# Kernel tuning notes

Measured on AMD Instinct MI355X. Metric: run time of the kernel, lower is better.

## Reference

```python
import jax, jax.numpy as jnp
import numpy as np

N_NODES = 20000
N_EDGES = 640000
NODE_DIM = 128
EDGE_DIM = 64
HID = 128  # must equal NODE_DIM (index_add_ into zeros_like(node_feat) in the original)
EPS = 1e-8


def setup_inputs() -> dict:
    key = jax.random.key(0)
    ks = jax.random.split(key, 16)
    s = 0.05
    return {
        "node_feat": jax.random.normal(ks[0], (N_NODES, NODE_DIM), jnp.float32),
        "edge_index": jax.random.randint(ks[1], (2, N_EDGES), 0, N_NODES, jnp.int32),
        "edge_attr": jax.random.normal(ks[2], (N_EDGES, EDGE_DIM), jnp.float32),
        "coords": jax.random.normal(ks[3], (N_NODES, 3), jnp.float32),
        # edge_mlp: Linear(2*node+edge -> hid), SiLU, Linear(hid -> hid), SiLU
        "eW1": jax.random.normal(ks[4], (2 * NODE_DIM + EDGE_DIM, HID), jnp.float32) * s,
        "eb1": jnp.zeros((HID,), jnp.float32),
        "eW2": jax.random.normal(ks[5], (HID, HID), jnp.float32) * s,
        "eb2": jnp.zeros((HID,), jnp.float32),
        # node_mlp: Linear(node+hid -> hid), SiLU, Linear(hid -> node)
        "nW1": jax.random.normal(ks[6], (NODE_DIM + HID, HID), jnp.float32) * s,
        "nb1": jnp.zeros((HID,), jnp.float32),
        "nW2": jax.random.normal(ks[7], (HID, NODE_DIM), jnp.float32) * s,
        "nb2": jnp.zeros((NODE_DIM,), jnp.float32),
        # coord_mlp: Linear(hid -> hid//2), SiLU, Linear(hid//2 -> 1)
        "cW1": jax.random.normal(ks[8], (HID, HID // 2), jnp.float32) * s,
        "cb1": jnp.zeros((HID // 2,), jnp.float32),
        "cW2": jax.random.normal(ks[9], (HID // 2, 1), jnp.float32) * s,
        "cb2": jnp.zeros((1,), jnp.float32),
    }


def reference(node_feat, edge_index, edge_attr, coords,
              eW1, eb1, eW2, eb2, nW1, nb1, nW2, nb2, cW1, cb1, cW2, cb2):
    silu = jax.nn.silu
    src, dst = edge_index[0], edge_index[1]

    # edge messages: gather -> concat -> 2-layer MLP (SiLU after both layers)
    edge_feat = jnp.concatenate([node_feat[src], node_feat[dst], edge_attr], axis=-1)  # [E, 2*node+edge]
    edge_message = silu(silu(edge_feat @ eW1 + eb1) @ eW2 + eb2)  # [E, hid]

    # aggregate messages per destination node (index_add_)
    aggr_message = jax.ops.segment_sum(edge_message, dst, num_segments=N_NODES)  # [N, hid]

    # node update (residual)
    node_input = jnp.concatenate([node_feat, aggr_message], axis=-1)
    node_update = silu(node_input @ nW1 + nb1) @ nW2 + nb2
    updated_nodes = node_feat + node_update

    # coordinate update: per-edge scalar weight times unit direction, scattered to dst
    coord_weights = silu(edge_message @ cW1 + cb1) @ cW2 + cb2  # [E, 1]
    coord_diff = coords[src] - coords[dst]  # [E, 3]
    coord_diff = coord_diff / (jnp.linalg.norm(coord_diff, axis=-1, keepdims=True) + EPS)
    coord_update = jax.ops.segment_sum(coord_weights * coord_diff, dst, num_segments=N_NODES)
    updated_coords = coords + coord_update

    return updated_nodes, updated_coords
```

## Files before the change

kernel.cpp:

```cpp
#include <hip/hip_runtime.h>
#include <math.h>

#define N_NODES 20000
#define N_EDGES 640000
#define D 128
#define ED 64
#define EPS 1e-8f
#define MT 64

#define FSTRIDE 328
#define HSTRIDE 136
#define MSG_OFF (MT * HSTRIDE)
#define LDS_SHORTS (MT * FSTRIDE)

#define NSTRIDE 264

#define EW2_OFF 40960
#define CW1_OFF 57344
#define NW1_OFF 65536
#define NW2_OFF 98304
#define NFBF_OFF 114688

typedef __attribute__((ext_vector_type(8))) short bf16x8;
typedef __attribute__((ext_vector_type(16))) float f32x16;
typedef __attribute__((ext_vector_type(2))) float f32x2;

__device__ __forceinline__ float silu_f(float x) { return x / (1.0f + __expf(-x)); }

__device__ __forceinline__ short f2bf(float f) {
    union { float f; unsigned u; } v; v.f = f;
    unsigned r = v.u + 0x7FFFu + ((v.u >> 16) & 1u);
    return (short)(r >> 16);
}
__device__ __forceinline__ float bf2f(short s) {
    union { unsigned u; float f; } v;
    v.u = ((unsigned)(unsigned short)s) << 16;
    return v.f;
}

#define SWZ_ADD(x, imm) (x + __int_as_float( \
    __builtin_amdgcn_ds_swizzle(__float_as_int(x), imm)))

__global__ __launch_bounds__(256)
void prep_kernel(const float* __restrict__ eW1, const float* __restrict__ eW2,
                 const float* __restrict__ cW1, const float* __restrict__ nW1,
                 const float* __restrict__ nW2,
                 const float* __restrict__ node_feat,
                 const float* __restrict__ coords,
                 short* __restrict__ wsf, short* __restrict__ nfbf,
                 float* __restrict__ nodes_io, float* __restrict__ out_coords) {
    const int t = blockIdx.x * blockDim.x + threadIdx.x;
    const int nthr = gridDim.x * blockDim.x;

    if (t < 224 * 64) {
        int f = t >> 6, lane = t & 63;
        const float* src; int kc, nt, ncol; size_t dst;
        if (f < 80)       {              src = eW1; kc = f >> 2;  nt = f & 3;  ncol = 128; dst = (size_t)f * 512; }
        else if (f < 112) { int g=f-80;  src = eW2; kc = g >> 2;  nt = g & 3;  ncol = 128; dst = EW2_OFF + (size_t)g * 512; }
        else if (f < 128) { int g=f-112; src = cW1; kc = g >> 1;  nt = g & 1;  ncol = 64;  dst = CW1_OFF + (size_t)g * 512; }
        else if (f < 192) { int g=f-128; src = nW1; kc = g >> 2;  nt = g & 3;  ncol = 128; dst = NW1_OFF + (size_t)g * 512; }
        else              { int g=f-192; src = nW2; kc = g >> 2;  nt = g & 3;  ncol = 128; dst = NW2_OFF + (size_t)g * 512; }
        int col = nt * 32 + (lane & 31);
        int k0  = kc * 16 + (lane >> 5) * 8;
        bf16x8 o;
        #pragma unroll
        for (int j = 0; j < 8; ++j) o[j] = f2bf(src[(size_t)(k0 + j) * ncol + col]);
        *(bf16x8*)&wsf[dst + (size_t)lane * 8] = o;
    }
    for (int idx = t; idx < N_NODES * D / 8; idx += nthr) {
        const float* s = node_feat + (size_t)idx * 8;
        float4 f0 = *(const float4*)s, f1 = *(const float4*)(s + 4);
        bf16x8 pk;
        pk[0]=f2bf(f0.x); pk[1]=f2bf(f0.y); pk[2]=f2bf(f0.z); pk[3]=f2bf(f0.w);
        pk[4]=f2bf(f1.x); pk[5]=f2bf(f1.y); pk[6]=f2bf(f1.z); pk[7]=f2bf(f1.w);
        *(bf16x8*)&nfbf[(size_t)idx * 8] = pk;
    }
    for (int idx = t; idx < N_NODES * D / 4; idx += nthr) {
        float4 z; z.x = 0.f; z.y = 0.f; z.z = 0.f; z.w = 0.f;
        *(float4*)&nodes_io[(size_t)idx * 4] = z;
    }
    for (int idx = t; idx < N_NODES * 3; idx += nthr)
        out_coords[idx] = coords[idx];
}

__global__ __launch_bounds__(256, 3)
void edge_kernel(const short* __restrict__ nfbf,
                 const int* __restrict__ edge_index,
                 const float* __restrict__ edge_attr,
                 const float* __restrict__ coords,
                 const float* __restrict__ eb1, const float* __restrict__ eb2,
                 const float* __restrict__ cb1, const float* __restrict__ cW2,
                 const float* __restrict__ cb2,
                 const short* __restrict__ wsf,
                 float* __restrict__ aggr_nodes, float* __restrict__ out_coords) {
    __shared__ __align__(16) short lds[LDS_SHORTS];
    __shared__ int s_src[MT], s_dst[MT];
    __shared__ float s_wgt[MT];

    const int tid = threadIdx.x;
    const int E0 = blockIdx.x * MT;

    {
        int e = tid >> 2, p = tid & 3;
        int esrc = edge_index[E0 + e];
        int edst = edge_index[N_EDGES + E0 + e];
        if (p == 0) { s_src[e] = esrc; s_dst[e] = edst; }
        const short* srow = nfbf + (size_t)esrc * D;
        const short* drow = nfbf + (size_t)edst * D;
        short* frow = &lds[e * FSTRIDE];
        #pragma unroll
        for (int c = 0; c < 4; ++c)
            *(bf16x8*)&frow[c * 32 + p * 8] = *(const bf16x8*)&srow[c * 32 + p * 8];
        #pragma unroll
        for (int c = 0; c < 4; ++c)
            *(bf16x8*)&frow[128 + c * 32 + p * 8] = *(const bf16x8*)&drow[c * 32 + p * 8];
        const float* arow = edge_attr + (size_t)(E0 + e) * ED + p * 16;
        float4 a0 = *(const float4*)&arow[0], a1 = *(const float4*)&arow[4];
        float4 a2 = *(const float4*)&arow[8], a3 = *(const float4*)&arow[12];
        bf16x8 p0, p1;
        p0[0]=f2bf(a0.x); p0[1]=f2bf(a0.y); p0[2]=f2bf(a0.z); p0[3]=f2bf(a0.w);
        p0[4]=f2bf(a1.x); p0[5]=f2bf(a1.y); p0[6]=f2bf(a1.z); p0[7]=f2bf(a1.w);
        p1[0]=f2bf(a2.x); p1[1]=f2bf(a2.y); p1[2]=f2bf(a2.z); p1[3]=f2bf(a2.w);
        p1[4]=f2bf(a3.x); p1[5]=f2bf(a3.y); p1[6]=f2bf(a3.z); p1[7]=f2bf(a3.w);
        *(bf16x8*)&frow[256 + p * 16]     = p0;
        *(bf16x8*)&frow[256 + p * 16 + 8] = p1;
    }
    __syncthreads();

    const int lane  = tid & 63;
    const int wv    = tid >> 6;
    const int m0    = (wv >> 1) * 32;
    const int n0q   = wv & 1;
    const int l31   = lane & 31;
    const int khalf = lane >> 5;

    const bf16x8* W1 = (const bf16x8*)wsf;
    const bf16x8* W2 = (const bf16x8*)(wsf + EW2_OFF);
    const bf16x8* W3 = (const bf16x8*)(wsf + CW1_OFF);

    {
        f32x16 acc0, acc1;
        #pragma unroll
        for (int r = 0; r < 16; ++r) { acc0[r] = 0.f; acc1[r] = 0.f; }
        #pragma unroll
        for (int kc = 0; kc < 20; ++kc) {
            bf16x8 a  = *(const bf16x8*)&lds[(m0 + l31) * FSTRIDE + kc * 16 + khalf * 8];
            bf16x8 b0 = W1[(kc * 4 + n0q * 2 + 0) * 64 + lane];
            bf16x8 b1 = W1[(kc * 4 + n0q * 2 + 1) * 64 + lane];
            acc0 = __builtin_amdgcn_mfma_f32_32x32x16_bf16(a, b0, acc0, 0, 0, 0);
            acc1 = __builtin_amdgcn_mfma_f32_32x32x16_bf16(a, b1, acc1, 0, 0, 0);
        }
        __syncthreads();
        #pragma unroll
        for (int nt = 0; nt < 2; ++nt) {
            f32x16 A = nt ? acc1 : acc0;
            int n = n0q * 64 + nt * 32 + l31;
            float bb = eb1[n];
            #pragma unroll
            for (int r = 0; r < 16; ++r) {
                int row = (r & 3) + 8 * (r >> 2) + 4 * khalf;
                lds[(m0 + row) * HSTRIDE + n] = f2bf(silu_f(A[r] + bb));
            }
        }
    }
    __syncthreads();

    {
        f32x16 acc0, acc1;
        #pragma unroll
        for (int r = 0; r < 16; ++r) { acc0[r] = 0.f; acc1[r] = 0.f; }
        #pragma unroll
        for (int kc = 0; kc < 8; ++kc) {
            bf16x8 a  = *(const bf16x8*)&lds[(m0 + l31) * HSTRIDE + kc * 16 + khalf * 8];
            bf16x8 b0 = W2[(kc * 4 + n0q * 2 + 0) * 64 + lane];
            bf16x8 b1 = W2[(kc * 4 + n0q * 2 + 1) * 64 + lane];
            acc0 = __builtin_amdgcn_mfma_f32_32x32x16_bf16(a, b0, acc0, 0, 0, 0);
            acc1 = __builtin_amdgcn_mfma_f32_32x32x16_bf16(a, b1, acc1, 0, 0, 0);
        }
        #pragma unroll
        for (int nt = 0; nt < 2; ++nt) {
            f32x16 A = nt ? acc1 : acc0;
            int n = n0q * 64 + nt * 32 + l31;
            float bb = eb2[n];
            #pragma unroll
            for (int r = 0; r < 16; ++r) {
                int row = (r & 3) + 8 * (r >> 2) + 4 * khalf;
                lds[MSG_OFF + (m0 + row) * HSTRIDE + n] = f2bf(silu_f(A[r] + bb));
            }
        }
    }
    __syncthreads();

    {
        f32x16 c0, c1;
        #pragma unroll
        for (int r = 0; r < 16; ++r) { c0[r] = 0.f; c1[r] = 0.f; }
        #pragma unroll
        for (int kc = 0; kc < 8; ++kc) {
            bf16x8 a  = *(const bf16x8*)&lds[MSG_OFF + (m0 + l31) * HSTRIDE + kc * 16 + khalf * 8];
            bf16x8 b0 = W3[(kc * 2 + 0) * 64 + lane];
            bf16x8 b1 = W3[(kc * 2 + 1) * 64 + lane];
            c0 = __builtin_amdgcn_mfma_f32_32x32x16_bf16(a, b0, c0, 0, 0, 0);
            c1 = __builtin_amdgcn_mfma_f32_32x32x16_bf16(a, b1, c1, 0, 0, 0);
        }
        float b1a = cb1[l31], b1b = cb1[32 + l31];
        float w2a = cW2[l31], w2b = cW2[32 + l31];
        float part[16];
        #pragma unroll
        for (int r = 0; r < 16; ++r)
            part[r] = silu_f(c0[r] + b1a) * w2a + silu_f(c1[r] + b1b) * w2b;
        #pragma unroll
        for (int r = 0; r < 16; ++r) {
            part[r] = SWZ_ADD(part[r], 0x041F);
            part[r] = SWZ_ADD(part[r], 0x081F);
            part[r] = SWZ_ADD(part[r], 0x101F);
            part[r] = SWZ_ADD(part[r], 0x201F);
            part[r] = SWZ_ADD(part[r], 0x401F);
        }
        if (l31 == 0) {
            float cb2v = cb2[0];
            #pragma unroll
            for (int r = 0; r < 16; ++r)
                s_wgt[m0 + (r & 3) + 8 * (r >> 2) + 4 * khalf] = part[r] + cb2v;
        }
    }
    __syncthreads();

    if (tid < MT) {
        int e = tid;
        float wgt = s_wgt[e];
        int s = s_src[e], d = s_dst[e];
        float dx = coords[s * 3 + 0] - coords[d * 3 + 0];
        float dy = coords[s * 3 + 1] - coords[d * 3 + 1];
        float dz = coords[s * 3 + 2] - coords[d * 3 + 2];
        float inv = wgt / (sqrtf(dx * dx + dy * dy + dz * dz) + EPS);
        unsafeAtomicAdd(&out_coords[d * 3 + 0], dx * inv);
        unsafeAtomicAdd(&out_coords[d * 3 + 1], dy * inv);
        unsafeAtomicAdd(&out_coords[d * 3 + 2], dz * inv);
    }

#if __has_builtin(__builtin_amdgcn_global_atomic_fadd_v2f32)
    for (int idx = tid; idx < MT * D / 8; idx += 256) {
        int e = idx >> 4, c = idx & 15;
        bf16x8 m = *(const bf16x8*)&lds[MSG_OFF + e * HSTRIDE + c * 8];
        float* ap = &aggr_nodes[(size_t)s_dst[e] * D + c * 8];
        #pragma unroll
        for (int j = 0; j < 4; ++j) {
            f32x2 v; v[0] = bf2f(m[2 * j]); v[1] = bf2f(m[2 * j + 1]);
            __builtin_amdgcn_global_atomic_fadd_v2f32((f32x2*)(ap + 2 * j), v);
        }
    }
#else
    for (int idx = tid; idx < MT * D; idx += 256) {
        int e = idx >> 7, n = idx & 127;
        float v = bf2f(lds[MSG_OFF + e * HSTRIDE + n]);
        unsafeAtomicAdd(&aggr_nodes[(size_t)s_dst[e] * D + n], v);
    }
#endif
}

__global__ __launch_bounds__(256, 4)
void node_kernel(const float* __restrict__ node_feat,
                 const short* __restrict__ nfbf,
                 float* nodes_io,
                 const float* __restrict__ nb1, const float* __restrict__ nb2,
                 const short* __restrict__ wsf) {
    __shared__ __align__(16) short lds[MT * NSTRIDE];
    const int tid = threadIdx.x;
    const int N0 = blockIdx.x * MT;

    {
        int i = tid >> 2, p = tid & 3;
        int nid = N0 + i; if (nid > N_NODES - 1) nid = N_NODES - 1;
        const short* frow = nfbf + (size_t)nid * D;
        short* drow = &lds[i * NSTRIDE];
        #pragma unroll
        for (int c = 0; c < 4; ++c)
            *(bf16x8*)&drow[c * 32 + p * 8] = *(const bf16x8*)&frow[c * 32 + p * 8];
        const float* arow = nodes_io + (size_t)nid * D + p * 32;
        #pragma unroll
        for (int c = 0; c < 4; ++c) {
            float4 f0 = *(const float4*)&arow[c * 8];
            float4 f1 = *(const float4*)&arow[c * 8 + 4];
            bf16x8 pk;
            pk[0]=f2bf(f0.x); pk[1]=f2bf(f0.y); pk[2]=f2bf(f0.z); pk[3]=f2bf(f0.w);
            pk[4]=f2bf(f1.x); pk[5]=f2bf(f1.y); pk[6]=f2bf(f1.z); pk[7]=f2bf(f1.w);
            *(bf16x8*)&drow[128 + p * 32 + c * 8] = pk;
        }
    }
    __syncthreads();

    const int lane  = tid & 63;
    const int wv    = tid >> 6;
    const int m0    = (wv >> 1) * 32;
    const int n0q   = wv & 1;
    const int l31   = lane & 31;
    const int khalf = lane >> 5;

    const bf16x8* W1 = (const bf16x8*)(wsf + NW1_OFF);
    const bf16x8* W2 = (const bf16x8*)(wsf + NW2_OFF);

    {
        f32x16 acc0, acc1;
        #pragma unroll
        for (int r = 0; r < 16; ++r) { acc0[r] = 0.f; acc1[r] = 0.f; }
        #pragma unroll
        for (int kc = 0; kc < 16; ++kc) {
            bf16x8 a  = *(const bf16x8*)&lds[(m0 + l31) * NSTRIDE + kc * 16 + khalf * 8];
            bf16x8 b0 = W1[(kc * 4 + n0q * 2 + 0) * 64 + lane];
            bf16x8 b1 = W1[(kc * 4 + n0q * 2 + 1) * 64 + lane];
            acc0 = __builtin_amdgcn_mfma_f32_32x32x16_bf16(a, b0, acc0, 0, 0, 0);
            acc1 = __builtin_amdgcn_mfma_f32_32x32x16_bf16(a, b1, acc1, 0, 0, 0);
        }
        __syncthreads();
        #pragma unroll
        for (int nt = 0; nt < 2; ++nt) {
            f32x16 A = nt ? acc1 : acc0;
            int n = n0q * 64 + nt * 32 + l31;
            float bb = nb1[n];
            #pragma unroll
            for (int r = 0; r < 16; ++r) {
                int row = (r & 3) + 8 * (r >> 2) + 4 * khalf;
                lds[(m0 + row) * HSTRIDE + n] = f2bf(silu_f(A[r] + bb));
            }
        }
    }
    __syncthreads();

    {
        f32x16 acc0, acc1;
        #pragma unroll
        for (int r = 0; r < 16; ++r) { acc0[r] = 0.f; acc1[r] = 0.f; }
        #pragma unroll
        for (int kc = 0; kc < 8; ++kc) {
            bf16x8 a  = *(const bf16x8*)&lds[(m0 + l31) * HSTRIDE + kc * 16 + khalf * 8];
            bf16x8 b0 = W2[(kc * 4 + n0q * 2 + 0) * 64 + lane];
            bf16x8 b1 = W2[(kc * 4 + n0q * 2 + 1) * 64 + lane];
            acc0 = __builtin_amdgcn_mfma_f32_32x32x16_bf16(a, b0, acc0, 0, 0, 0);
            acc1 = __builtin_amdgcn_mfma_f32_32x32x16_bf16(a, b1, acc1, 0, 0, 0);
        }
        #pragma unroll
        for (int nt = 0; nt < 2; ++nt) {
            f32x16 A = nt ? acc1 : acc0;
            int n = n0q * 64 + nt * 32 + l31;
            float bb = nb2[n];
            #pragma unroll
            for (int r = 0; r < 16; ++r) {
                int row = (r & 3) + 8 * (r >> 2) + 4 * khalf;
                int nid = N0 + m0 + row;
                if (nid < N_NODES)
                    nodes_io[(size_t)nid * D + n] = A[r] + bb + node_feat[(size_t)nid * D + n];
            }
        }
    }
}

extern "C" void kernel_launch(void* const* d_in, const int* in_sizes, int n_in,
                              void* d_out, int out_size, void* d_ws, size_t ws_size,
                              hipStream_t stream) {
    const float* node_feat  = (const float*)d_in[0];
    const int*   edge_index = (const int*)d_in[1];
    const float* edge_attr  = (const float*)d_in[2];
    const float* coords     = (const float*)d_in[3];
    const float* eW1 = (const float*)d_in[4];
    const float* eb1 = (const float*)d_in[5];
    const float* eW2 = (const float*)d_in[6];
    const float* eb2 = (const float*)d_in[7];
    const float* nW1 = (const float*)d_in[8];
    const float* nb1 = (const float*)d_in[9];
    const float* nW2 = (const float*)d_in[10];
    const float* nb2 = (const float*)d_in[11];
    const float* cW1 = (const float*)d_in[12];
    const float* cb1 = (const float*)d_in[13];
    const float* cW2 = (const float*)d_in[14];
    const float* cb2 = (const float*)d_in[15];

    float* nodes_io   = (float*)d_out;
    float* out_coords = nodes_io + (size_t)N_NODES * D;
    short* wsf  = (short*)d_ws;
    short* nfbf = wsf + NFBF_OFF;

    prep_kernel<<<256, 256, 0, stream>>>(
        eW1, eW2, cW1, nW1, nW2, node_feat, coords,
        wsf, nfbf, nodes_io, out_coords);
    edge_kernel<<<N_EDGES / MT, 256, 0, stream>>>(
        nfbf, edge_index, edge_attr, coords,
        eb1, eb2, cb1, cW2, cb2, wsf, nodes_io, out_coords);
    node_kernel<<<(N_NODES + MT - 1) / MT, 256, 0, stream>>>(
        node_feat, nfbf, nodes_io, nb1, nb2, wsf);
}
```

Measured before the change: 635.1 us.

## Sort edges by destination and pre-reduce segments before atomic scatter

Adds a counting sort of edges by destination node: a histogram pass, a single-block scan and a scatter that builds a permutation. The edge kernel then processes edges in destination order and reduces runs of equal destination within each 64-edge tile before issuing atomics, for both node messages and coordinate updates. With about 32 edges per node, this should cut global atomic traffic substantially. The cost is three extra kernel launches, a serial one-block scan, gathered edge_attr reads through the permutation, and scalar atomics replacing the packed v2 atomics.

```diff
diff --git a/kernel.cpp b/kernel.cpp
--- a/kernel.cpp
+++ b/kernel.cpp
@@ -20,10 +20,11 @@
 #define NW1_OFF 65536
 #define NW2_OFF 98304
 #define NFBF_OFF 114688
+#define CSR_OFF  2674688
 
 typedef __attribute__((ext_vector_type(8))) short bf16x8;
+typedef __attribute__((ext_vector_type(4))) short bf16x4;
 typedef __attribute__((ext_vector_type(16))) float f32x16;
-typedef __attribute__((ext_vector_type(2))) float f32x2;
 
 __device__ __forceinline__ float silu_f(float x) { return x / (1.0f + __expf(-x)); }
 
@@ -48,6 +49,7 @@
                  const float* __restrict__ node_feat,
                  const float* __restrict__ coords,
                  short* __restrict__ wsf, short* __restrict__ nfbf,
+                 int* __restrict__ cnt,
                  float* __restrict__ nodes_io, float* __restrict__ out_coords) {
     const int t = blockIdx.x * blockDim.x + threadIdx.x;
     const int nthr = gridDim.x * blockDim.x;
@@ -79,13 +81,61 @@
         float4 z; z.x = 0.f; z.y = 0.f; z.z = 0.f; z.w = 0.f;
         *(float4*)&nodes_io[(size_t)idx * 4] = z;
     }
+    for (int idx = t; idx < N_NODES; idx += nthr) cnt[idx] = 0;
     for (int idx = t; idx < N_NODES * 3; idx += nthr)
         out_coords[idx] = coords[idx];
+}
+
+__global__ __launch_bounds__(256)
+void hist_kernel(const int* __restrict__ edge_index, int* __restrict__ cnt) {
+    int t = blockIdx.x * blockDim.x + threadIdx.x;
+    if (t < N_EDGES) atomicAdd(&cnt[edge_index[N_EDGES + t]], 1);
+}
+
+#define SCAN_T 1024
+#define SCAN_C 20
+__global__ __launch_bounds__(SCAN_T)
+void scan_kernel(const int* __restrict__ cnt, int* __restrict__ cursor) {
+    __shared__ int part[SCAN_T];
+    const int t = threadIdx.x;
+    const int base = t * SCAN_C;
+    int s = 0;
+    #pragma unroll
+    for (int i = 0; i < SCAN_C; ++i) {
+        int idx = base + i;
+        if (idx < N_NODES) s += cnt[idx];
+    }
+    part[t] = s;
+    __syncthreads();
+    for (int off = 1; off < SCAN_T; off <<= 1) {
+        int v = (t >= off) ? part[t - off] : 0;
+        __syncthreads();
+        part[t] += v;
+        __syncthreads();
+    }
+    int run = part[t] - s;
+    #pragma unroll
+    for (int i = 0; i < SCAN_C; ++i) {
+        int idx = base + i;
+        if (idx < N_NODES) { cursor[idx] = run; run += cnt[idx]; }
+    }
+}
+
+__global__ __launch_bounds__(256)
+void scatter_kernel(const int* __restrict__ edge_index,
+                    int* __restrict__ cursor, int* __restrict__ perm) {
+    int t = blockIdx.x * blockDim.x + threadIdx.x;
+    if (t < N_EDGES) {
+        int d = edge_index[N_EDGES + t];
+        int pos = atomicAdd(&cursor[d], 1);
+        perm[pos] = t;
+    }
 }
 
 __global__ __launch_bounds__(256, 3)
 void edge_kernel(const short* __restrict__ nfbf,
                  const int* __restrict__ edge_index,
+                 const int* __restrict__ perm,
                  const float* __restrict__ edge_attr,
                  const float* __restrict__ coords,
                  const float* __restrict__ eb1, const float* __restrict__ eb2,
@@ -96,25 +146,28 @@
     __shared__ __align__(16) short lds[LDS_SHORTS];
     __shared__ int s_src[MT], s_dst[MT];
     __shared__ float s_wgt[MT];
+    __shared__ float s_cv[MT][3];
+    __shared__ char s_segend[MT];
 
     const int tid = threadIdx.x;
     const int E0 = blockIdx.x * MT;
 
     {
-        int e = tid >> 2, p = tid & 3;
-        int esrc = edge_index[E0 + e];
-        int edst = edge_index[N_EDGES + E0 + e];
-        if (p == 0) { s_src[e] = esrc; s_dst[e] = edst; }
+        int i = tid >> 2, p = tid & 3;
+        int eid  = perm[E0 + i];
+        int esrc = edge_index[eid];
+        int edst = edge_index[N_EDGES + eid];
+        if (p == 0) { s_src[i] = esrc; s_dst[i] = edst; }
         const short* srow = nfbf + (size_t)esrc * D;
         const short* drow = nfbf + (size_t)edst * D;
-        short* frow = &lds[e * FSTRIDE];
+        short* frow = &lds[i * FSTRIDE];
         #pragma unroll
         for (int c = 0; c < 4; ++c)
             *(bf16x8*)&frow[c * 32 + p * 8] = *(const bf16x8*)&srow[c * 32 + p * 8];
         #pragma unroll
         for (int c = 0; c < 4; ++c)
             *(bf16x8*)&frow[128 + c * 32 + p * 8] = *(const bf16x8*)&drow[c * 32 + p * 8];
-        const float* arow = edge_attr + (size_t)(E0 + e) * ED + p * 16;
+        const float* arow = edge_attr + (size_t)eid * ED + p * 16;
         float4 a0 = *(const float4*)&arow[0], a1 = *(const float4*)&arow[4];
         float4 a2 = *(const float4*)&arow[8], a3 = *(const float4*)&arow[12];
         bf16x8 p0, p1;
@@ -127,6 +180,9 @@
     }
     __syncthreads();
 
+    if (tid < MT)
+        s_segend[tid] = (tid == MT - 1) || (s_dst[tid] != s_dst[tid + 1]);
+
     const int lane  = tid & 63;
     const int wv    = tid >> 6;
     const int m0    = (wv >> 1) * 32;
@@ -234,29 +290,51 @@
         float dy = coords[s * 3 + 1] - coords[d * 3 + 1];
         float dz = coords[s * 3 + 2] - coords[d * 3 + 2];
         float inv = wgt / (sqrtf(dx * dx + dy * dy + dz * dz) + EPS);
-        unsafeAtomicAdd(&out_coords[d * 3 + 0], dx * inv);
-        unsafeAtomicAdd(&out_coords[d * 3 + 1], dy * inv);
-        unsafeAtomicAdd(&out_coords[d * 3 + 2], dz * inv);
-    }
-
-#if __has_builtin(__builtin_amdgcn_global_atomic_fadd_v2f32)
-    for (int idx = tid; idx < MT * D / 8; idx += 256) {
-        int e = idx >> 4, c = idx & 15;
-        bf16x8 m = *(const bf16x8*)&lds[MSG_OFF + e * HSTRIDE + c * 8];
-        float* ap = &aggr_nodes[(size_t)s_dst[e] * D + c * 8];
-        #pragma unroll
-        for (int j = 0; j < 4; ++j) {
-            f32x2 v; v[0] = bf2f(m[2 * j]); v[1] = bf2f(m[2 * j + 1]);
-            __builtin_amdgcn_global_atomic_fadd_v2f32((f32x2*)(ap + 2 * j), v);
-        }
-    }
-#else
-    for (int idx = tid; idx < MT * D; idx += 256) {
-        int e = idx >> 7, n = idx & 127;
-        float v = bf2f(lds[MSG_OFF + e * HSTRIDE + n]);
-        unsafeAtomicAdd(&aggr_nodes[(size_t)s_dst[e] * D + n], v);
-    }
-#endif
+        s_cv[e][0] = dx * inv; s_cv[e][1] = dy * inv; s_cv[e][2] = dz * inv;
+    }
+    __syncthreads();
+
+    {
+        int q  = tid & 31;
+        int st = tid >> 5;
+        int c0 = q * 4;
+        float a0 = 0.f, a1 = 0.f, a2 = 0.f, a3 = 0.f;
+        #pragma unroll
+        for (int r = 0; r < 8; ++r) {
+            int e = st * 8 + r;
+            bf16x4 m = *(const bf16x4*)&lds[MSG_OFF + e * HSTRIDE + c0];
+            a0 += bf2f(m[0]); a1 += bf2f(m[1]); a2 += bf2f(m[2]); a3 += bf2f(m[3]);
+            if (s_segend[e]) {
+                float* ap = &aggr_nodes[(size_t)s_dst[e] * D + c0];
+                unsafeAtomicAdd(ap + 0, a0); unsafeAtomicAdd(ap + 1, a1);
+                unsafeAtomicAdd(ap + 2, a2); unsafeAtomicAdd(ap + 3, a3);
+                a0 = a1 = a2 = a3 = 0.f;
+            }
+        }
+        int elast = st * 8 + 7;
+        if (!s_segend[elast]) {
+            float* ap = &aggr_nodes[(size_t)s_dst[elast] * D + c0];
+            unsafeAtomicAdd(ap + 0, a0); unsafeAtomicAdd(ap + 1, a1);
+            unsafeAtomicAdd(ap + 2, a2); unsafeAtomicAdd(ap + 3, a3);
+        }
+    }
+
+    if (tid < MT) {
+        int e = tid;
+        bool head = (e == 0) || (s_dst[e] != s_dst[e - 1]);
+        if (head) {
+            float sx = 0.f, sy = 0.f, sz = 0.f;
+            int j = e;
+            do {
+                sx += s_cv[j][0]; sy += s_cv[j][1]; sz += s_cv[j][2];
+                ++j;
+            } while (j < MT && s_dst[j] == s_dst[e]);
+            int d = s_dst[e];
+            unsafeAtomicAdd(&out_coords[d * 3 + 0], sx);
+            unsafeAtomicAdd(&out_coords[d * 3 + 1], sy);
+            unsafeAtomicAdd(&out_coords[d * 3 + 2], sz);
+        }
+    }
 }
 
 __global__ __launch_bounds__(256, 4)
@@ -377,14 +455,20 @@
 
     float* nodes_io   = (float*)d_out;
     float* out_coords = nodes_io + (size_t)N_NODES * D;
-    short* wsf  = (short*)d_ws;
-    short* nfbf = wsf + NFBF_OFF;
+    short* wsf    = (short*)d_ws;
+    short* nfbf   = wsf + NFBF_OFF;
+    int*   cnt    = (int*)(wsf + CSR_OFF);
+    int*   cursor = cnt + N_NODES;
+    int*   perm   = cursor + N_NODES;
 
     prep_kernel<<<256, 256, 0, stream>>>(
         eW1, eW2, cW1, nW1, nW2, node_feat, coords,
-        wsf, nfbf, nodes_io, out_coords);
+        wsf, nfbf, cnt, nodes_io, out_coords);
+    hist_kernel<<<N_EDGES / 256, 256, 0, stream>>>(edge_index, cnt);
+    scan_kernel<<<1, SCAN_T, 0, stream>>>(cnt, cursor);
+    scatter_kernel<<<N_EDGES / 256, 256, 0, stream>>>(edge_index, cursor, perm);
     edge_kernel<<<N_EDGES / MT, 256, 0, stream>>>(
-        nfbf, edge_index, edge_attr, coords,
+        nfbf, edge_index, perm, edge_attr, coords,
         eb1, eb2, cb1, cW2, cb2, wsf, nodes_io, out_coords);
     node_kernel<<<(N_NODES + MT - 1) / MT, 256, 0, stream>>>(
         node_feat, nfbf, nodes_io, nb1, nb2, wsf);
```

Result: faster. 618.8 us (-2.6%).
